# Kernel tuning notes

Measured on AMD Instinct MI355X. Metric: run time of the kernel, lower is better.

## Reference

```python
import jax, jax.numpy as jnp
import numpy as np

B, N, P, H = 32, 64, 4, 300  # batch, nodes, node properties, glove hidden size


def setup_inputs() -> dict:
    key = jax.random.key(0)
    ks = jax.random.split(key, 6)
    return {
        "node_attr": jax.random.normal(ks[0], (B, N, P, H), jnp.float32),
        "edge_attr": jax.random.normal(ks[1], (B, N, N, H), jnp.float32),
        "instruction": jax.random.normal(ks[2], (B, H), jnp.float32),
        "distribution": jax.random.uniform(ks[3], (B, N), jnp.float32),
        "node_prop_similarities": jax.random.uniform(ks[4], (B, P), jnp.float32),
        "relation_prop_similarity": jax.random.uniform(ks[5], (B,), jnp.float32),
        "node_mask": jnp.zeros((B, N), jnp.float32),
        # learned parameters, initialized exactly as the torch module does
        "weight_node_properties": jnp.tile(jnp.eye(H, dtype=jnp.float32)[None], (P, 1, 1)),
        "weight_edge": jnp.eye(H, dtype=jnp.float32),
        "weight_state_score": jnp.ones((H,), jnp.float32),
        "weight_relation_score": jnp.ones((H,), jnp.float32),
    }


def reference(node_attr, edge_attr, instruction, distribution,
              node_prop_similarities, relation_prop_similarity, node_mask,
              weight_node_properties, weight_edge,
              weight_state_score, weight_relation_score):
    # node_scores: ELU( sum_p nps[b,p] * instr[b,k] * (node_attr[b,:,p,:] @ W_p)[b,p,n,k] )  -> B,N,H
    # (dropout p=0.0 -> identity)
    node_scores = jax.nn.elu(
        jnp.einsum('bnph,phk,bk,bp->bnk',
                   node_attr, weight_node_properties,
                   instruction, node_prop_similarities))
    # edge_scores: ELU( instr[b,k] * (edge_attr @ W_edge) )  -> B,N,N,H (materialized, like the original)
    edge_scores = jax.nn.elu(
        jnp.einsum('bmnh,hk,bk->bmnk', edge_attr, weight_edge, instruction))
    # state logits: node_scores @ w_state + mask  -> B,N
    state_logits = jnp.einsum('bnk,k->bn', node_scores, weight_state_score) + node_mask
    # relation logits: (sum_n edge_scores[b,m,n,:] * dist[b,n]) @ w_rel + mask -> B,N
    rel_logits = jnp.einsum('bmnk,bn,k->bm',
                            edge_scores, distribution, weight_relation_score) + node_mask
    dist_states = jax.nn.softmax(state_logits, axis=1)
    dist_relations = jax.nn.softmax(rel_logits, axis=1)
    r = relation_prop_similarity[:, None]  # B,1
    return r * dist_relations + (1.0 - r) * dist_states
```

## Files before the change

### kernel.cpp

```cpp
#include <hip/hip_runtime.h>
#include <math.h>

#define BB 32
#define NN 64
#define PP 4
#define HH 300

#define NKK 10
#define NCT 19
#define NCTE 20
#define NPAIR 10
#define NKK2 38
#define CHK 10

#define NODE_BLOCKS (BB * 4)
#define EDGE_BLOCKS (BB * NN / 2)

typedef float    f32x4 __attribute__((ext_vector_type(4)));
typedef _Float16 f16x8 __attribute__((ext_vector_type(8)));

__device__ __forceinline__ float eluf(float x) {
    return x > 0.0f ? x : (__expf(x) - 1.0f);
}

extern "C" __global__ __launch_bounds__(64)
void wprep_kernel(const float* __restrict__ w_edge,
                  const float* __restrict__ w_np,
                  _Float16* __restrict__ w_hi,
                  _Float16* __restrict__ w2_hi)
{
    const int lane = (int)threadIdx.x;
    int bid = (int)blockIdx.x;
    if (bid < NKK * NCTE) {
        const int kk = bid / NCTE, ct = bid % NCTE;
        const int h0 = kk * 32 + (lane >> 4) * 8;
        const int k  = ct * 16 + (lane & 15);
        const size_t base = ((size_t)bid * 64 + lane) * 8;
#pragma unroll
        for (int j = 0; j < 8; ++j) {
            int h = h0 + j;
            float v = (h < HH && k < HH) ? w_edge[h * HH + k] : 0.f;
            w_hi[base + j] = (_Float16)v;
        }
    } else {
        bid -= NKK * NCTE;
        const int kk = bid / NCT, ct = bid % NCT;
        const int h0 = kk * 32 + (lane >> 4) * 8;
        const int k  = ct * 16 + (lane & 15);
        const size_t base = ((size_t)bid * 64 + lane) * 8;
#pragma unroll
        for (int j = 0; j < 8; ++j) {
            int h = h0 + j;
            float v = (h < PP * HH && k < HH) ? w_np[(size_t)h * HH + k] : 0.f;
            w2_hi[base + j] = (_Float16)v;
        }
    }
}

extern "C" __global__ __launch_bounds__(256)
void fused_kernel(const float* __restrict__ edge_attr,
                  const float* __restrict__ node_attr,
                  const float* __restrict__ instr,
                  const float* __restrict__ dist,
                  const float* __restrict__ sim,
                  const float* __restrict__ node_mask,
                  const _Float16* __restrict__ w_hi,
                  const _Float16* __restrict__ w2_hi,
                  const float* __restrict__ w_rel,
                  const float* __restrict__ w_state,
                  float* __restrict__ rel_logits,
                  float* __restrict__ state_logits)
{
    __shared__ __align__(16) _Float16 Bs[2 * NKK * 512];
    __shared__ float redE[2][NN];
    __shared__ float redN[4][16];
    const int tid  = (int)threadIdx.x;
    const int wv   = tid >> 6;
    const int lane = tid & 63;
    const int lrow = lane & 15;
    const int lgrp = lane >> 4;

    if ((int)blockIdx.x < NODE_BLOCKS) {
        const int bid = (int)blockIdx.x;
        const int b   = bid >> 2;
        const int nt  = bid & 3;

        const float* arow = node_attr
            + (size_t)(b * NN + nt * 16 + lrow) * (PP * HH);
        float sm[PP];
#pragma unroll
        for (int p = 0; p < PP; ++p) sm[p] = sim[b * PP + p];

        const f16x8* WH = reinterpret_cast<const f16x8*>(w2_hi);

        f32x4 acc[5] = {{0.f,0.f,0.f,0.f},{0.f,0.f,0.f,0.f},{0.f,0.f,0.f,0.f},
                        {0.f,0.f,0.f,0.f},{0.f,0.f,0.f,0.f}};

#pragma unroll 1
        for (int ch = 0; ch < 4; ++ch) {
            f16x8 a_h[CHK];
#pragma unroll
            for (int q = 0; q < CHK; ++q) {
                const int kk = ch * CHK + q;
                const int h0 = kk * 32 + lgrp * 8;
                float v[8];
                if (kk < NKK2 && h0 + 7 < PP * HH) {
                    f32x4 p0 = *reinterpret_cast<const f32x4*>(arow + h0);
                    f32x4 p1 = *reinterpret_cast<const f32x4*>(arow + h0 + 4);
                    v[0] = p0[0]; v[1] = p0[1]; v[2] = p0[2]; v[3] = p0[3];
                    v[4] = p1[0]; v[5] = p1[1]; v[6] = p1[2]; v[7] = p1[3];
                } else {
#pragma unroll
                    for (int j = 0; j < 8; ++j)
                        v[j] = (kk < NKK2 && h0 + j < PP * HH) ? arow[h0 + j] : 0.f;
                }
#pragma unroll
                for (int j = 0; j < 8; ++j) {
                    const int h = h0 + j;
                    const int p = (h < PP * HH) ? (h / HH) : 0;
                    a_h[q][j] = (_Float16)(v[j] * sm[p]);
                }
            }
#pragma unroll
            for (int q = 0; q < CHK; ++q) {
                const int kk = ch * CHK + q;
                if (kk < NKK2) {
#pragma unroll
                    for (int c = 0; c < 5; ++c) {
                        const int ct = wv + 4 * c;
                        if (ct < NCT) {
                            f16x8 bh = WH[(kk * NCT + ct) * 64 + lane];
                            acc[c] = __builtin_amdgcn_mfma_f32_16x16x32_f16(a_h[q], bh, acc[c], 0, 0, 0);
                        }
                    }
                }
            }
        }

        float rs0 = 0.f, rs1 = 0.f, rs2 = 0.f, rs3 = 0.f;
#pragma unroll
        for (int c = 0; c < 5; ++c) {
            const int ct = wv + 4 * c;
            if (ct < NCT) {
                const int k  = ct * 16 + lrow;
                const bool ok = k < HH;
                const int kc = ok ? k : (HH - 1);
                const float iv  = instr[b * HH + kc];
                const float wsv = ok ? w_state[kc] : 0.f;
                rs0 += eluf(acc[c][0] * iv) * wsv;
                rs1 += eluf(acc[c][1] * iv) * wsv;
                rs2 += eluf(acc[c][2] * iv) * wsv;
                rs3 += eluf(acc[c][3] * iv) * wsv;
            }
        }
#pragma unroll
        for (int msk = 1; msk < 16; msk <<= 1) {
            rs0 += __shfl_xor(rs0, msk);
            rs1 += __shfl_xor(rs1, msk);
            rs2 += __shfl_xor(rs2, msk);
            rs3 += __shfl_xor(rs3, msk);
        }
        if (lrow == 0) {
            redN[wv][lgrp * 4 + 0] = rs0;
            redN[wv][lgrp * 4 + 1] = rs1;
            redN[wv][lgrp * 4 + 2] = rs2;
            redN[wv][lgrp * 4 + 3] = rs3;
        }
        __syncthreads();
        if (tid < 16) {
            const int n = nt * 16 + tid;
            float v = redN[0][tid] + redN[1][tid] + redN[2][tid] + redN[3][tid];
            state_logits[b * NN + n] = v + node_mask[b * NN + n];
        }
        return;
    }

    const int ebid = (int)blockIdx.x - NODE_BLOCKS;
    const int b    = ebid / (NN / 2);
    const int mp   = ebid % (NN / 2);
    const int m0   = 2 * mp;
    const int mi   = wv >> 1;
    const int rh   = wv & 1;

    const float* abase = edge_attr
        + (size_t)((b * NN + m0 + mi) * NN + rh * 32 + lrow) * HH;
    f16x8 aA[NKK], aB[NKK];
#pragma unroll
    for (int s = 0; s < 2; ++s) {
        const float* arow = abase + (size_t)(s * 16) * HH;
#pragma unroll
        for (int kk = 0; kk < NKK; ++kk) {
            const int h0 = kk * 32 + lgrp * 8;
            float v[8];
            if (h0 + 7 < HH) {
                f32x4 p0 = *reinterpret_cast<const f32x4*>(arow + h0);
                f32x4 p1 = *reinterpret_cast<const f32x4*>(arow + h0 + 4);
                v[0] = p0[0]; v[1] = p0[1]; v[2] = p0[2]; v[3] = p0[3];
                v[4] = p1[0]; v[5] = p1[1]; v[6] = p1[2]; v[7] = p1[3];
            } else {
#pragma unroll
                for (int j = 0; j < 8; ++j)
                    v[j] = (h0 + j < HH) ? arow[h0 + j] : 0.f;
            }
            if (s == 0) {
#pragma unroll
                for (int j = 0; j < 8; ++j) aA[kk][j] = (_Float16)v[j];
            } else {
#pragma unroll
                for (int j = 0; j < 8; ++j) aB[kk][j] = (_Float16)v[j];
            }
        }
    }

    const f16x8* WH = reinterpret_cast<const f16x8*>(w_hi);
    const int binst = b * HH;

    const int t0 = wv * 5;
    const f16x8* gp[5];
    int ldst[5];
#pragma unroll
    for (int i = 0; i < 5; ++i) {
        int t  = t0 + i;
        int c  = (t >= NKK) ? 1 : 0;
        int kk = t - c * NKK;
        gp[i]   = WH + ((size_t)kk * NCTE + c) * 64 + lane;
        ldst[i] = (c * NKK + kk) * 512 + lane * 8;
    }

    f16x8 st[5];
#pragma unroll
    for (int i = 0; i < 5; ++i) { st[i] = gp[i][0]; gp[i] += 128; }

    float rsA0 = 0.f, rsA1 = 0.f, rsA2 = 0.f, rsA3 = 0.f;
    float rsB0 = 0.f, rsB1 = 0.f, rsB2 = 0.f, rsB3 = 0.f;

#pragma unroll 1
    for (int p = 0; p < NPAIR; ++p) {
#pragma unroll
        for (int i = 0; i < 5; ++i)
            *reinterpret_cast<f16x8*>(&Bs[ldst[i]]) = st[i];
        __syncthreads();

        if (p + 1 < NPAIR) {
#pragma unroll
            for (int i = 0; i < 5; ++i) { st[i] = gp[i][0]; gp[i] += 128; }
        }

        f32x4 accA0 = {0.f, 0.f, 0.f, 0.f};
        f32x4 accA1 = {0.f, 0.f, 0.f, 0.f};
        f32x4 accB0 = {0.f, 0.f, 0.f, 0.f};
        f32x4 accB1 = {0.f, 0.f, 0.f, 0.f};
        const _Float16* bsc = &Bs[lane * 8];
#pragma unroll
        for (int kk = 0; kk < NKK; ++kk) {
            f16x8 b0 = *reinterpret_cast<const f16x8*>(bsc + kk * 512);
            f16x8 b1 = *reinterpret_cast<const f16x8*>(bsc + (NKK + kk) * 512);
            accA0 = __builtin_amdgcn_mfma_f32_16x16x32_f16(aA[kk], b0, accA0, 0, 0, 0);
            accB0 = __builtin_amdgcn_mfma_f32_16x16x32_f16(aB[kk], b0, accB0, 0, 0, 0);
            accA1 = __builtin_amdgcn_mfma_f32_16x16x32_f16(aA[kk], b1, accA1, 0, 0, 0);
            accB1 = __builtin_amdgcn_mfma_f32_16x16x32_f16(aB[kk], b1, accB1, 0, 0, 0);
        }

#pragma unroll
        for (int c = 0; c < 2; ++c) {
            const int k  = (2 * p + c) * 16 + lrow;
            const bool ok = k < HH;
            const int kc = ok ? k : (HH - 1);
            const float iv = instr[binst + kc];
            const float wr = ok ? w_rel[kc] : 0.f;
            const f32x4 aAc = c ? accA1 : accA0;
            const f32x4 aBc = c ? accB1 : accB0;
            rsA0 += eluf(aAc[0] * iv) * wr;
            rsA1 += eluf(aAc[1] * iv) * wr;
            rsA2 += eluf(aAc[2] * iv) * wr;
            rsA3 += eluf(aAc[3] * iv) * wr;
            rsB0 += eluf(aBc[0] * iv) * wr;
            rsB1 += eluf(aBc[1] * iv) * wr;
            rsB2 += eluf(aBc[2] * iv) * wr;
            rsB3 += eluf(aBc[3] * iv) * wr;
        }

        __syncthreads();
    }

#pragma unroll
    for (int msk = 1; msk < 16; msk <<= 1) {
        rsA0 += __shfl_xor(rsA0, msk);
        rsA1 += __shfl_xor(rsA1, msk);
        rsA2 += __shfl_xor(rsA2, msk);
        rsA3 += __shfl_xor(rsA3, msk);
        rsB0 += __shfl_xor(rsB0, msk);
        rsB1 += __shfl_xor(rsB1, msk);
        rsB2 += __shfl_xor(rsB2, msk);
        rsB3 += __shfl_xor(rsB3, msk);
    }
    if (lrow == 0) {
        const int r0 = rh * 32 + lgrp * 4;
        redE[mi][r0 + 0]      = rsA0;
        redE[mi][r0 + 1]      = rsA1;
        redE[mi][r0 + 2]      = rsA2;
        redE[mi][r0 + 3]      = rsA3;
        redE[mi][r0 + 16 + 0] = rsB0;
        redE[mi][r0 + 16 + 1] = rsB1;
        redE[mi][r0 + 16 + 2] = rsB2;
        redE[mi][r0 + 16 + 3] = rsB3;
    }
    __syncthreads();
    if (tid < 128) {
        const int mm = tid >> 6;
        const int ln = tid & 63;
        float v = redE[mm][ln] * dist[b * NN + ln];
#pragma unroll
        for (int msk = 1; msk < 64; msk <<= 1) v += __shfl_xor(v, msk);
        if (ln == 0)
            rel_logits[b * NN + m0 + mm] = v + node_mask[b * NN + m0 + mm];
    }
}

extern "C" __global__ __launch_bounds__(64)
void final_kernel(const float* __restrict__ rel_logits,
                  const float* __restrict__ state_logits,
                  const float* __restrict__ rel_sim,
                  float* __restrict__ out)
{
    const int b = (int)blockIdx.x;
    const int n = (int)threadIdx.x;
    float sl = state_logits[b * NN + n];
    float rl = rel_logits[b * NN + n];

    float ms = sl, mr = rl;
#pragma unroll
    for (int msk = 1; msk < 64; msk <<= 1) {
        ms = fmaxf(ms, __shfl_xor(ms, msk));
        mr = fmaxf(mr, __shfl_xor(mr, msk));
    }
    float es = __expf(sl - ms);
    float er = __expf(rl - mr);
    float ss = es, sr = er;
#pragma unroll
    for (int msk = 1; msk < 64; msk <<= 1) {
        ss += __shfl_xor(ss, msk);
        sr += __shfl_xor(sr, msk);
    }
    float rr = rel_sim[b];
    out[b * NN + n] = rr * (er / sr) + (1.f - rr) * (es / ss);
}

extern "C" void kernel_launch(void* const* d_in, const int* in_sizes, int n_in,
                              void* d_out, int out_size, void* d_ws, size_t ws_size,
                              hipStream_t stream) {
    const float* node_attr    = (const float*)d_in[0];
    const float* edge_attr    = (const float*)d_in[1];
    const float* instruction  = (const float*)d_in[2];
    const float* distribution = (const float*)d_in[3];
    const float* node_sim     = (const float*)d_in[4];
    const float* rel_sim      = (const float*)d_in[5];
    const float* node_mask    = (const float*)d_in[6];
    const float* w_np         = (const float*)d_in[7];
    const float* w_edge       = (const float*)d_in[8];
    const float* w_state      = (const float*)d_in[9];
    const float* w_rel        = (const float*)d_in[10];
    float* out = (float*)d_out;

    float* rel_ws   = (float*)d_ws;
    float* state_ws = rel_ws + BB * NN;
    char*  wsb      = (char*)d_ws;
    const size_t edge_frag = (size_t)NKK * NCTE * 64 * 8 * 2;
    _Float16* w_hi  = (_Float16*)(wsb + 16384);
    _Float16* w2_hi = (_Float16*)(wsb + 16384 + edge_frag);

    wprep_kernel<<<dim3(NKK * NCTE + NKK2 * NCT), dim3(64), 0, stream>>>(
        w_edge, w_np, w_hi, w2_hi);

    fused_kernel<<<dim3(NODE_BLOCKS + EDGE_BLOCKS), dim3(256), 0, stream>>>(
        edge_attr, node_attr, instruction, distribution, node_sim, node_mask,
        w_hi, w2_hi, w_rel, w_state, rel_ws, state_ws);

    final_kernel<<<dim3(BB), dim3(64), 0, stream>>>(
        rel_ws, state_ws, rel_sim, out);
}
```

Before: 82.35 us.

## Stage edge tile through LDS with coalesced loads, one m row per block

```diff
diff --git a/kernel.cpp b/kernel.cpp
--- a/kernel.cpp
+++ b/kernel.cpp
@@ -14,10 +14,12 @@
 #define CHK 10
 
 #define NODE_BLOCKS (BB * 4)
-#define EDGE_BLOCKS (BB * NN / 2)
+#define EDGE_BLOCKS (BB * NN)
+#define ASTR 344
 
 typedef float    f32x4 __attribute__((ext_vector_type(4)));
 typedef _Float16 f16x8 __attribute__((ext_vector_type(8)));
+typedef _Float16 f16x4 __attribute__((ext_vector_type(4)));
 
 __device__ __forceinline__ float eluf(float x) {
     return x > 0.0f ? x : (__expf(x) - 1.0f);
@@ -71,8 +73,9 @@
                   float* __restrict__ rel_logits,
                   float* __restrict__ state_logits)
 {
+    __shared__ __align__(16) _Float16 As[NN * ASTR];
     __shared__ __align__(16) _Float16 Bs[2 * NKK * 512];
-    __shared__ float redE[2][NN];
+    __shared__ float redE[NN];
     __shared__ float redN[4][16];
     const int tid  = (int)threadIdx.x;
     const int wv   = tid >> 6;
@@ -176,40 +179,38 @@
     }
 
     const int ebid = (int)blockIdx.x - NODE_BLOCKS;
-    const int b    = ebid / (NN / 2);
-    const int mp   = ebid % (NN / 2);
-    const int m0   = 2 * mp;
-    const int mi   = wv >> 1;
-    const int rh   = wv & 1;
-
-    const float* abase = edge_attr
-        + (size_t)((b * NN + m0 + mi) * NN + rh * 32 + lrow) * HH;
-    f16x8 aA[NKK], aB[NKK];
-#pragma unroll
-    for (int s = 0; s < 2; ++s) {
-        const float* arow = abase + (size_t)(s * 16) * HH;
-#pragma unroll
-        for (int kk = 0; kk < NKK; ++kk) {
-            const int h0 = kk * 32 + lgrp * 8;
-            float v[8];
-            if (h0 + 7 < HH) {
-                f32x4 p0 = *reinterpret_cast<const f32x4*>(arow + h0);
-                f32x4 p1 = *reinterpret_cast<const f32x4*>(arow + h0 + 4);
-                v[0] = p0[0]; v[1] = p0[1]; v[2] = p0[2]; v[3] = p0[3];
-                v[4] = p1[0]; v[5] = p1[1]; v[6] = p1[2]; v[7] = p1[3];
-            } else {
-#pragma unroll
-                for (int j = 0; j < 8; ++j)
-                    v[j] = (h0 + j < HH) ? arow[h0 + j] : 0.f;
-            }
-            if (s == 0) {
-#pragma unroll
-                for (int j = 0; j < 8; ++j) aA[kk][j] = (_Float16)v[j];
-            } else {
-#pragma unroll
-                for (int j = 0; j < 8; ++j) aB[kk][j] = (_Float16)v[j];
-            }
-        }
+    const int b    = ebid / NN;
+    const int m    = ebid % NN;
+
+    {
+        const float* asrc = edge_attr + (size_t)(b * NN + m) * (NN * HH);
+#pragma unroll 1
+        for (int q = tid; q < NN * HH / 4; q += 256) {
+            f32x4 v = *reinterpret_cast<const f32x4*>(asrc + q * 4);
+            const int row = q / 75;
+            const int cq  = q - row * 75;
+            f16x4 h;
+            h[0] = (_Float16)v[0]; h[1] = (_Float16)v[1];
+            h[2] = (_Float16)v[2]; h[3] = (_Float16)v[3];
+            *reinterpret_cast<f16x4*>(&As[row * ASTR + cq * 4]) = h;
+        }
+        f16x4 z = {(_Float16)0.f, (_Float16)0.f, (_Float16)0.f, (_Float16)0.f};
+#pragma unroll 1
+        for (int i = tid; i < NN * 5; i += 256) {
+            const int row = i / 5;
+            const int j   = i - row * 5;
+            *reinterpret_cast<f16x4*>(&As[row * ASTR + 300 + j * 4]) = z;
+        }
+    }
+    __syncthreads();
+
+    f16x8 aA[NKK];
+    {
+        const int arow_l = wv * 16 + lrow;
+#pragma unroll
+        for (int kk = 0; kk < NKK; ++kk)
+            aA[kk] = *reinterpret_cast<const f16x8*>(
+                &As[arow_l * ASTR + kk * 32 + lgrp * 8]);
     }
 
     const f16x8* WH = reinterpret_cast<const f16x8*>(w_hi);
@@ -231,8 +232,7 @@
 #pragma unroll
     for (int i = 0; i < 5; ++i) { st[i] = gp[i][0]; gp[i] += 128; }
 
-    float rsA0 = 0.f, rsA1 = 0.f, rsA2 = 0.f, rsA3 = 0.f;
-    float rsB0 = 0.f, rsB1 = 0.f, rsB2 = 0.f, rsB3 = 0.f;
+    float rs0 = 0.f, rs1 = 0.f, rs2 = 0.f, rs3 = 0.f;
 
 #pragma unroll 1
     for (int p = 0; p < NPAIR; ++p) {
@@ -246,19 +246,15 @@
             for (int i = 0; i < 5; ++i) { st[i] = gp[i][0]; gp[i] += 128; }
         }
 
-        f32x4 accA0 = {0.f, 0.f, 0.f, 0.f};
-        f32x4 accA1 = {0.f, 0.f, 0.f, 0.f};
-        f32x4 accB0 = {0.f, 0.f, 0.f, 0.f};
-        f32x4 accB1 = {0.f, 0.f, 0.f, 0.f};
+        f32x4 acc0 = {0.f, 0.f, 0.f, 0.f};
+        f32x4 acc1 = {0.f, 0.f, 0.f, 0.f};
         const _Float16* bsc = &Bs[lane * 8];
 #pragma unroll
         for (int kk = 0; kk < NKK; ++kk) {
             f16x8 b0 = *reinterpret_cast<const f16x8*>(bsc + kk * 512);
             f16x8 b1 = *reinterpret_cast<const f16x8*>(bsc + (NKK + kk) * 512);
-            accA0 = __builtin_amdgcn_mfma_f32_16x16x32_f16(aA[kk], b0, accA0, 0, 0, 0);
-            accB0 = __builtin_amdgcn_mfma_f32_16x16x32_f16(aB[kk], b0, accB0, 0, 0, 0);
-            accA1 = __builtin_amdgcn_mfma_f32_16x16x32_f16(aA[kk], b1, accA1, 0, 0, 0);
-            accB1 = __builtin_amdgcn_mfma_f32_16x16x32_f16(aB[kk], b1, accB1, 0, 0, 0);
+            acc0 = __builtin_amdgcn_mfma_f32_16x16x32_f16(aA[kk], b0, acc0, 0, 0, 0);
+            acc1 = __builtin_amdgcn_mfma_f32_16x16x32_f16(aA[kk], b1, acc1, 0, 0, 0);
         }
 
 #pragma unroll
@@ -268,16 +264,11 @@
             const int kc = ok ? k : (HH - 1);
             const float iv = instr[binst + kc];
             const float wr = ok ? w_rel[kc] : 0.f;
-            const f32x4 aAc = c ? accA1 : accA0;
-            const f32x4 aBc = c ? accB1 : accB0;
-            rsA0 += eluf(aAc[0] * iv) * wr;
-            rsA1 += eluf(aAc[1] * iv) * wr;
-            rsA2 += eluf(aAc[2] * iv) * wr;
-            rsA3 += eluf(aAc[3] * iv) * wr;
-            rsB0 += eluf(aBc[0] * iv) * wr;
-            rsB1 += eluf(aBc[1] * iv) * wr;
-            rsB2 += eluf(aBc[2] * iv) * wr;
-            rsB3 += eluf(aBc[3] * iv) * wr;
+            const f32x4 ac = c ? acc1 : acc0;
+            rs0 += eluf(ac[0] * iv) * wr;
+            rs1 += eluf(ac[1] * iv) * wr;
+            rs2 += eluf(ac[2] * iv) * wr;
+            rs3 += eluf(ac[3] * iv) * wr;
         }
 
         __syncthreads();
@@ -285,35 +276,25 @@
 
 #pragma unroll
     for (int msk = 1; msk < 16; msk <<= 1) {
-        rsA0 += __shfl_xor(rsA0, msk);
-        rsA1 += __shfl_xor(rsA1, msk);
-        rsA2 += __shfl_xor(rsA2, msk);
-        rsA3 += __shfl_xor(rsA3, msk);
-        rsB0 += __shfl_xor(rsB0, msk);
-        rsB1 += __shfl_xor(rsB1, msk);
-        rsB2 += __shfl_xor(rsB2, msk);
-        rsB3 += __shfl_xor(rsB3, msk);
+        rs0 += __shfl_xor(rs0, msk);
+        rs1 += __shfl_xor(rs1, msk);
+        rs2 += __shfl_xor(rs2, msk);
+        rs3 += __shfl_xor(rs3, msk);
     }
     if (lrow == 0) {
-        const int r0 = rh * 32 + lgrp * 4;
-        redE[mi][r0 + 0]      = rsA0;
-        redE[mi][r0 + 1]      = rsA1;
-        redE[mi][r0 + 2]      = rsA2;
-        redE[mi][r0 + 3]      = rsA3;
-        redE[mi][r0 + 16 + 0] = rsB0;
-        redE[mi][r0 + 16 + 1] = rsB1;
-        redE[mi][r0 + 16 + 2] = rsB2;
-        redE[mi][r0 + 16 + 3] = rsB3;
+        const int r0 = wv * 16 + lgrp * 4;
+        redE[r0 + 0] = rs0;
+        redE[r0 + 1] = rs1;
+        redE[r0 + 2] = rs2;
+        redE[r0 + 3] = rs3;
     }
     __syncthreads();
-    if (tid < 128) {
-        const int mm = tid >> 6;
-        const int ln = tid & 63;
-        float v = redE[mm][ln] * dist[b * NN + ln];
+    if (tid < 64) {
+        float v = redE[tid] * dist[b * NN + tid];
 #pragma unroll
         for (int msk = 1; msk < 64; msk <<= 1) v += __shfl_xor(v, msk);
-        if (ln == 0)
-            rel_logits[b * NN + m0 + mm] = v + node_mask[b * NN + m0 + mm];
+        if (tid == 0)
+            rel_logits[b * NN + m] = v + node_mask[b * NN + m];
     }
 }
 
```

Result: slower. 99.90 us (+21.3%).

## Fuse softmax finalization into main kernel via per-batch last-block counter

Applied to the files above, without the earlier changes.

```diff
diff --git a/kernel.cpp b/kernel.cpp
--- a/kernel.cpp
+++ b/kernel.cpp
@@ -15,6 +15,8 @@
 
 #define NODE_BLOCKS (BB * 4)
 #define EDGE_BLOCKS (BB * NN / 2)
+#define BLOCKS_PER_B 36
+#define NTILES (NKK * NCTE + NKK2 * NCT)
 
 typedef float    f32x4 __attribute__((ext_vector_type(4)));
 typedef _Float16 f16x8 __attribute__((ext_vector_type(8)));
@@ -23,19 +25,20 @@
     return x > 0.0f ? x : (__expf(x) - 1.0f);
 }
 
-extern "C" __global__ __launch_bounds__(64)
+extern "C" __global__ __launch_bounds__(256)
 void wprep_kernel(const float* __restrict__ w_edge,
                   const float* __restrict__ w_np,
                   _Float16* __restrict__ w_hi,
                   _Float16* __restrict__ w2_hi)
 {
-    const int lane = (int)threadIdx.x;
-    int bid = (int)blockIdx.x;
-    if (bid < NKK * NCTE) {
-        const int kk = bid / NCTE, ct = bid % NCTE;
+    const int lane = (int)threadIdx.x & 63;
+    int tile = (int)blockIdx.x * 4 + ((int)threadIdx.x >> 6);
+    if (tile >= NTILES) return;
+    if (tile < NKK * NCTE) {
+        const int kk = tile / NCTE, ct = tile % NCTE;
         const int h0 = kk * 32 + (lane >> 4) * 8;
         const int k  = ct * 16 + (lane & 15);
-        const size_t base = ((size_t)bid * 64 + lane) * 8;
+        const size_t base = ((size_t)tile * 64 + lane) * 8;
 #pragma unroll
         for (int j = 0; j < 8; ++j) {
             int h = h0 + j;
@@ -43,11 +46,11 @@
             w_hi[base + j] = (_Float16)v;
         }
     } else {
-        bid -= NKK * NCTE;
-        const int kk = bid / NCT, ct = bid % NCT;
+        tile -= NKK * NCTE;
+        const int kk = tile / NCT, ct = tile % NCT;
         const int h0 = kk * 32 + (lane >> 4) * 8;
         const int k  = ct * 16 + (lane & 15);
-        const size_t base = ((size_t)bid * 64 + lane) * 8;
+        const size_t base = ((size_t)tile * 64 + lane) * 8;
 #pragma unroll
         for (int j = 0; j < 8; ++j) {
             int h = h0 + j;
@@ -68,22 +71,28 @@
                   const _Float16* __restrict__ w2_hi,
                   const float* __restrict__ w_rel,
                   const float* __restrict__ w_state,
+                  const float* __restrict__ rel_sim,
                   float* __restrict__ rel_logits,
-                  float* __restrict__ state_logits)
+                  float* __restrict__ state_logits,
+                  int* __restrict__ cnt,
+                  float* __restrict__ out)
 {
     __shared__ __align__(16) _Float16 Bs[2 * NKK * 512];
     __shared__ float redE[2][NN];
     __shared__ float redN[4][16];
+    __shared__ int lastFlag;
     const int tid  = (int)threadIdx.x;
     const int wv   = tid >> 6;
     const int lane = tid & 63;
     const int lrow = lane & 15;
     const int lgrp = lane >> 4;
+    int bfin;
 
     if ((int)blockIdx.x < NODE_BLOCKS) {
         const int bid = (int)blockIdx.x;
         const int b   = bid >> 2;
         const int nt  = bid & 3;
+        bfin = b;
 
         const float* arow = node_attr
             + (size_t)(b * NN + nt * 16 + lrow) * (PP * HH);
@@ -169,181 +178,188 @@
         __syncthreads();
         if (tid < 16) {
             const int n = nt * 16 + tid;
-            float v = redN[0][tid] + redN[1][tid] + redN[2][tid] + redN[3][tid];
-            state_logits[b * NN + n] = v + node_mask[b * NN + n];
-        }
-        return;
+            float v = redN[0][tid] + redN[1][tid] + redN[2][tid] + redN[3][tid]
+                      + node_mask[b * NN + n];
+            __hip_atomic_store(&state_logits[b * NN + n], v,
+                               __ATOMIC_RELEASE, __HIP_MEMORY_SCOPE_AGENT);
+        }
+    } else {
+        const int ebid = (int)blockIdx.x - NODE_BLOCKS;
+        const int b    = ebid / (NN / 2);
+        const int mp   = ebid % (NN / 2);
+        const int m0   = 2 * mp;
+        const int mi   = wv >> 1;
+        const int rh   = wv & 1;
+        bfin = b;
+
+        const float* abase = edge_attr
+            + (size_t)((b * NN + m0 + mi) * NN + rh * 32 + lrow) * HH;
+        f16x8 aA[NKK], aB[NKK];
+#pragma unroll
+        for (int s = 0; s < 2; ++s) {
+            const float* arow = abase + (size_t)(s * 16) * HH;
+#pragma unroll
+            for (int kk = 0; kk < NKK; ++kk) {
+                const int h0 = kk * 32 + lgrp * 8;
+                float v[8];
+                if (h0 + 7 < HH) {
+                    f32x4 p0 = *reinterpret_cast<const f32x4*>(arow + h0);
+                    f32x4 p1 = *reinterpret_cast<const f32x4*>(arow + h0 + 4);
+                    v[0] = p0[0]; v[1] = p0[1]; v[2] = p0[2]; v[3] = p0[3];
+                    v[4] = p1[0]; v[5] = p1[1]; v[6] = p1[2]; v[7] = p1[3];
+                } else {
+#pragma unroll
+                    for (int j = 0; j < 8; ++j)
+                        v[j] = (h0 + j < HH) ? arow[h0 + j] : 0.f;
+                }
+                if (s == 0) {
+#pragma unroll
+                    for (int j = 0; j < 8; ++j) aA[kk][j] = (_Float16)v[j];
+                } else {
+#pragma unroll
+                    for (int j = 0; j < 8; ++j) aB[kk][j] = (_Float16)v[j];
+                }
+            }
+        }
+
+        const f16x8* WH = reinterpret_cast<const f16x8*>(w_hi);
+        const int binst = b * HH;
+
+        const int t0 = wv * 5;
+        const f16x8* gp[5];
+        int ldst[5];
+#pragma unroll
+        for (int i = 0; i < 5; ++i) {
+            int t  = t0 + i;
+            int c  = (t >= NKK) ? 1 : 0;
+            int kk = t - c * NKK;
+            gp[i]   = WH + ((size_t)kk * NCTE + c) * 64 + lane;
+            ldst[i] = (c * NKK + kk) * 512 + lane * 8;
+        }
+
+        f16x8 st[5];
+#pragma unroll
+        for (int i = 0; i < 5; ++i) { st[i] = gp[i][0]; gp[i] += 128; }
+
+        float rsA0 = 0.f, rsA1 = 0.f, rsA2 = 0.f, rsA3 = 0.f;
+        float rsB0 = 0.f, rsB1 = 0.f, rsB2 = 0.f, rsB3 = 0.f;
+
+#pragma unroll 1
+        for (int p = 0; p < NPAIR; ++p) {
+#pragma unroll
+            for (int i = 0; i < 5; ++i)
+                *reinterpret_cast<f16x8*>(&Bs[ldst[i]]) = st[i];
+            __syncthreads();
+
+            if (p + 1 < NPAIR) {
+#pragma unroll
+                for (int i = 0; i < 5; ++i) { st[i] = gp[i][0]; gp[i] += 128; }
+            }
+
+            f32x4 accA0 = {0.f, 0.f, 0.f, 0.f};
+            f32x4 accA1 = {0.f, 0.f, 0.f, 0.f};
+            f32x4 accB0 = {0.f, 0.f, 0.f, 0.f};
+            f32x4 accB1 = {0.f, 0.f, 0.f, 0.f};
+            const _Float16* bsc = &Bs[lane * 8];
+#pragma unroll
+            for (int kk = 0; kk < NKK; ++kk) {
+                f16x8 b0 = *reinterpret_cast<const f16x8*>(bsc + kk * 512);
+                f16x8 b1 = *reinterpret_cast<const f16x8*>(bsc + (NKK + kk) * 512);
+                accA0 = __builtin_amdgcn_mfma_f32_16x16x32_f16(aA[kk], b0, accA0, 0, 0, 0);
+                accB0 = __builtin_amdgcn_mfma_f32_16x16x32_f16(aB[kk], b0, accB0, 0, 0, 0);
+                accA1 = __builtin_amdgcn_mfma_f32_16x16x32_f16(aA[kk], b1, accA1, 0, 0, 0);
+                accB1 = __builtin_amdgcn_mfma_f32_16x16x32_f16(aB[kk], b1, accB1, 0, 0, 0);
+            }
+
+#pragma unroll
+            for (int c = 0; c < 2; ++c) {
+                const int k  = (2 * p + c) * 16 + lrow;
+                const bool ok = k < HH;
+                const int kc = ok ? k : (HH - 1);
+                const float iv = instr[binst + kc];
+                const float wr = ok ? w_rel[kc] : 0.f;
+                const f32x4 aAc = c ? accA1 : accA0;
+                const f32x4 aBc = c ? accB1 : accB0;
+                rsA0 += eluf(aAc[0] * iv) * wr;
+                rsA1 += eluf(aAc[1] * iv) * wr;
+                rsA2 += eluf(aAc[2] * iv) * wr;
+                rsA3 += eluf(aAc[3] * iv) * wr;
+                rsB0 += eluf(aBc[0] * iv) * wr;
+                rsB1 += eluf(aBc[1] * iv) * wr;
+                rsB2 += eluf(aBc[2] * iv) * wr;
+                rsB3 += eluf(aBc[3] * iv) * wr;
+            }
+
+            __syncthreads();
+        }
+
+#pragma unroll
+        for (int msk = 1; msk < 16; msk <<= 1) {
+            rsA0 += __shfl_xor(rsA0, msk);
+            rsA1 += __shfl_xor(rsA1, msk);
+            rsA2 += __shfl_xor(rsA2, msk);
+            rsA3 += __shfl_xor(rsA3, msk);
+            rsB0 += __shfl_xor(rsB0, msk);
+            rsB1 += __shfl_xor(rsB1, msk);
+            rsB2 += __shfl_xor(rsB2, msk);
+            rsB3 += __shfl_xor(rsB3, msk);
+        }
+        if (lrow == 0) {
+            const int r0 = rh * 32 + lgrp * 4;
+            redE[mi][r0 + 0]      = rsA0;
+            redE[mi][r0 + 1]      = rsA1;
+            redE[mi][r0 + 2]      = rsA2;
+            redE[mi][r0 + 3]      = rsA3;
+            redE[mi][r0 + 16 + 0] = rsB0;
+            redE[mi][r0 + 16 + 1] = rsB1;
+            redE[mi][r0 + 16 + 2] = rsB2;
+            redE[mi][r0 + 16 + 3] = rsB3;
+        }
+        __syncthreads();
+        if (tid < 128) {
+            const int mm = tid >> 6;
+            const int ln = tid & 63;
+            float v = redE[mm][ln] * dist[b * NN + ln];
+#pragma unroll
+            for (int msk = 1; msk < 64; msk <<= 1) v += __shfl_xor(v, msk);
+            if (ln == 0) {
+                float lv = v + node_mask[b * NN + m0 + mm];
+                __hip_atomic_store(&rel_logits[b * NN + m0 + mm], lv,
+                                   __ATOMIC_RELEASE, __HIP_MEMORY_SCOPE_AGENT);
+            }
+        }
     }
 
-    const int ebid = (int)blockIdx.x - NODE_BLOCKS;
-    const int b    = ebid / (NN / 2);
-    const int mp   = ebid % (NN / 2);
-    const int m0   = 2 * mp;
-    const int mi   = wv >> 1;
-    const int rh   = wv & 1;
-
-    const float* abase = edge_attr
-        + (size_t)((b * NN + m0 + mi) * NN + rh * 32 + lrow) * HH;
-    f16x8 aA[NKK], aB[NKK];
-#pragma unroll
-    for (int s = 0; s < 2; ++s) {
-        const float* arow = abase + (size_t)(s * 16) * HH;
-#pragma unroll
-        for (int kk = 0; kk < NKK; ++kk) {
-            const int h0 = kk * 32 + lgrp * 8;
-            float v[8];
-            if (h0 + 7 < HH) {
-                f32x4 p0 = *reinterpret_cast<const f32x4*>(arow + h0);
-                f32x4 p1 = *reinterpret_cast<const f32x4*>(arow + h0 + 4);
-                v[0] = p0[0]; v[1] = p0[1]; v[2] = p0[2]; v[3] = p0[3];
-                v[4] = p1[0]; v[5] = p1[1]; v[6] = p1[2]; v[7] = p1[3];
-            } else {
-#pragma unroll
-                for (int j = 0; j < 8; ++j)
-                    v[j] = (h0 + j < HH) ? arow[h0 + j] : 0.f;
-            }
-            if (s == 0) {
-#pragma unroll
-                for (int j = 0; j < 8; ++j) aA[kk][j] = (_Float16)v[j];
-            } else {
-#pragma unroll
-                for (int j = 0; j < 8; ++j) aB[kk][j] = (_Float16)v[j];
-            }
-        }
-    }
-
-    const f16x8* WH = reinterpret_cast<const f16x8*>(w_hi);
-    const int binst = b * HH;
-
-    const int t0 = wv * 5;
-    const f16x8* gp[5];
-    int ldst[5];
-#pragma unroll
-    for (int i = 0; i < 5; ++i) {
-        int t  = t0 + i;
-        int c  = (t >= NKK) ? 1 : 0;
-        int kk = t - c * NKK;
-        gp[i]   = WH + ((size_t)kk * NCTE + c) * 64 + lane;
-        ldst[i] = (c * NKK + kk) * 512 + lane * 8;
-    }
-
-    f16x8 st[5];
-#pragma unroll
-    for (int i = 0; i < 5; ++i) { st[i] = gp[i][0]; gp[i] += 128; }
-
-    float rsA0 = 0.f, rsA1 = 0.f, rsA2 = 0.f, rsA3 = 0.f;
-    float rsB0 = 0.f, rsB1 = 0.f, rsB2 = 0.f, rsB3 = 0.f;
-
-#pragma unroll 1
-    for (int p = 0; p < NPAIR; ++p) {
-#pragma unroll
-        for (int i = 0; i < 5; ++i)
-            *reinterpret_cast<f16x8*>(&Bs[ldst[i]]) = st[i];
-        __syncthreads();
-
-        if (p + 1 < NPAIR) {
-#pragma unroll
-            for (int i = 0; i < 5; ++i) { st[i] = gp[i][0]; gp[i] += 128; }
-        }
-
-        f32x4 accA0 = {0.f, 0.f, 0.f, 0.f};
-        f32x4 accA1 = {0.f, 0.f, 0.f, 0.f};
-        f32x4 accB0 = {0.f, 0.f, 0.f, 0.f};
-        f32x4 accB1 = {0.f, 0.f, 0.f, 0.f};
-        const _Float16* bsc = &Bs[lane * 8];
-#pragma unroll
-        for (int kk = 0; kk < NKK; ++kk) {
-            f16x8 b0 = *reinterpret_cast<const f16x8*>(bsc + kk * 512);
-            f16x8 b1 = *reinterpret_cast<const f16x8*>(bsc + (NKK + kk) * 512);
-            accA0 = __builtin_amdgcn_mfma_f32_16x16x32_f16(aA[kk], b0, accA0, 0, 0, 0);
-            accB0 = __builtin_amdgcn_mfma_f32_16x16x32_f16(aB[kk], b0, accB0, 0, 0, 0);
-            accA1 = __builtin_amdgcn_mfma_f32_16x16x32_f16(aA[kk], b1, accA1, 0, 0, 0);
-            accB1 = __builtin_amdgcn_mfma_f32_16x16x32_f16(aB[kk], b1, accB1, 0, 0, 0);
-        }
-
-#pragma unroll
-        for (int c = 0; c < 2; ++c) {
-            const int k  = (2 * p + c) * 16 + lrow;
-            const bool ok = k < HH;
-            const int kc = ok ? k : (HH - 1);
-            const float iv = instr[binst + kc];
-            const float wr = ok ? w_rel[kc] : 0.f;
-            const f32x4 aAc = c ? accA1 : accA0;
-            const f32x4 aBc = c ? accB1 : accB0;
-            rsA0 += eluf(aAc[0] * iv) * wr;
-            rsA1 += eluf(aAc[1] * iv) * wr;
-            rsA2 += eluf(aAc[2] * iv) * wr;
-            rsA3 += eluf(aAc[3] * iv) * wr;
-            rsB0 += eluf(aBc[0] * iv) * wr;
-            rsB1 += eluf(aBc[1] * iv) * wr;
-            rsB2 += eluf(aBc[2] * iv) * wr;
-            rsB3 += eluf(aBc[3] * iv) * wr;
-        }
-
-        __syncthreads();
-    }
-
-#pragma unroll
-    for (int msk = 1; msk < 16; msk <<= 1) {
-        rsA0 += __shfl_xor(rsA0, msk);
-        rsA1 += __shfl_xor(rsA1, msk);
-        rsA2 += __shfl_xor(rsA2, msk);
-        rsA3 += __shfl_xor(rsA3, msk);
-        rsB0 += __shfl_xor(rsB0, msk);
-        rsB1 += __shfl_xor(rsB1, msk);
-        rsB2 += __shfl_xor(rsB2, msk);
-        rsB3 += __shfl_xor(rsB3, msk);
-    }
-    if (lrow == 0) {
-        const int r0 = rh * 32 + lgrp * 4;
-        redE[mi][r0 + 0]      = rsA0;
-        redE[mi][r0 + 1]      = rsA1;
-        redE[mi][r0 + 2]      = rsA2;
-        redE[mi][r0 + 3]      = rsA3;
-        redE[mi][r0 + 16 + 0] = rsB0;
-        redE[mi][r0 + 16 + 1] = rsB1;
-        redE[mi][r0 + 16 + 2] = rsB2;
-        redE[mi][r0 + 16 + 3] = rsB3;
+    if (tid == 0) {
+        int old = __hip_atomic_fetch_add(&cnt[bfin], 1,
+                                         __ATOMIC_ACQ_REL,
+                                         __HIP_MEMORY_SCOPE_AGENT);
+        lastFlag = (old == BLOCKS_PER_B - 1) ? 1 : 0;
     }
     __syncthreads();
-    if (tid < 128) {
-        const int mm = tid >> 6;
-        const int ln = tid & 63;
-        float v = redE[mm][ln] * dist[b * NN + ln];
-#pragma unroll
-        for (int msk = 1; msk < 64; msk <<= 1) v += __shfl_xor(v, msk);
-        if (ln == 0)
-            rel_logits[b * NN + m0 + mm] = v + node_mask[b * NN + m0 + mm];
+    if (lastFlag && tid < 64) {
+        const int n = tid;
+        float sl = __hip_atomic_load(&state_logits[bfin * NN + n],
+                                     __ATOMIC_ACQUIRE, __HIP_MEMORY_SCOPE_AGENT);
+        float rl = __hip_atomic_load(&rel_logits[bfin * NN + n],
+                                     __ATOMIC_ACQUIRE, __HIP_MEMORY_SCOPE_AGENT);
+        float ms = sl, mr = rl;
+#pragma unroll
+        for (int msk = 1; msk < 64; msk <<= 1) {
+            ms = fmaxf(ms, __shfl_xor(ms, msk));
+            mr = fmaxf(mr, __shfl_xor(mr, msk));
+        }
+        float es = __expf(sl - ms);
+        float er = __expf(rl - mr);
+        float ss = es, sr = er;
+#pragma unroll
+        for (int msk = 1; msk < 64; msk <<= 1) {
+            ss += __shfl_xor(ss, msk);
+            sr += __shfl_xor(sr, msk);
+        }
+        float rr = rel_sim[bfin];
+        out[bfin * NN + n] = rr * (er / sr) + (1.f - rr) * (es / ss);
     }
-}
-
-extern "C" __global__ __launch_bounds__(64)
-void final_kernel(const float* __restrict__ rel_logits,
-                  const float* __restrict__ state_logits,
-                  const float* __restrict__ rel_sim,
-                  float* __restrict__ out)
-{
-    const int b = (int)blockIdx.x;
-    const int n = (int)threadIdx.x;
-    float sl = state_logits[b * NN + n];
-    float rl = rel_logits[b * NN + n];
-
-    float ms = sl, mr = rl;
-#pragma unroll
-    for (int msk = 1; msk < 64; msk <<= 1) {
-        ms = fmaxf(ms, __shfl_xor(ms, msk));
-        mr = fmaxf(mr, __shfl_xor(mr, msk));
-    }
-    float es = __expf(sl - ms);
-    float er = __expf(rl - mr);
-    float ss = es, sr = er;
-#pragma unroll
-    for (int msk = 1; msk < 64; msk <<= 1) {
-        ss += __shfl_xor(ss, msk);
-        sr += __shfl_xor(sr, msk);
-    }
-    float rr = rel_sim[b];
-    out[b * NN + n] = rr * (er / sr) + (1.f - rr) * (es / ss);
 }
 
 extern "C" void kernel_launch(void* const* d_in, const int* in_sizes, int n_in,
@@ -362,20 +378,20 @@
     const float* w_rel        = (const float*)d_in[10];
     float* out = (float*)d_out;
 
-    float* rel_ws   = (float*)d_ws;
+    char*  wsb      = (char*)d_ws;
+    float* rel_ws   = (float*)wsb;
     float* state_ws = rel_ws + BB * NN;
-    char*  wsb      = (char*)d_ws;
+    int*   cnt      = (int*)(wsb + 16384);
     const size_t edge_frag = (size_t)NKK * NCTE * 64 * 8 * 2;
-    _Float16* w_hi  = (_Float16*)(wsb + 16384);
-    _Float16* w2_hi = (_Float16*)(wsb + 16384 + edge_frag);
-
-    wprep_kernel<<<dim3(NKK * NCTE + NKK2 * NCT), dim3(64), 0, stream>>>(
+    _Float16* w_hi  = (_Float16*)(wsb + 16640);
+    _Float16* w2_hi = (_Float16*)(wsb + 16640 + edge_frag);
+
+    hipMemsetAsync(cnt, 0, BB * sizeof(int), stream);
+
+    wprep_kernel<<<dim3((NTILES + 3) / 4), dim3(256), 0, stream>>>(
         w_edge, w_np, w_hi, w2_hi);
 
     fused_kernel<<<dim3(NODE_BLOCKS + EDGE_BLOCKS), dim3(256), 0, stream>>>(
         edge_attr, node_attr, instruction, distribution, node_sim, node_mask,
-        w_hi, w2_hi, w_rel, w_state, rel_ws, state_ws);
-
-    final_kernel<<<dim3(BB), dim3(64), 0, stream>>>(
-        rel_ws, state_ws, rel_sim, out);
+        w_hi, w2_hi, w_rel, w_state, rel_sim, rel_ws, state_ws, cnt, out);
 }
```

After: 135.6 us. 1.65x slower.
